# Performance work log

Measured on AMD Instinct MI355X. Metric: run time of the kernel, lower is better.

## Reference

```python
import jax, jax.numpy as jnp
import numpy as np

VOCAB = 100000
EMB = 100
HID = 100
CTX_LEN = 60          # must equal MAX_DESC_LEN for linear_1 to fit
FACT_LEN = 20
DESC_LEN = 60


def setup_inputs() -> dict:
    key = jax.random.key(0)
    ks = jax.random.split(key, 12)
    s = 0.05
    context = jax.random.randint(ks[0], (CTX_LEN, FACT_LEN), 1, VOCAB)
    fact_lengths = jax.random.randint(ks[1], (CTX_LEN,), 1, FACT_LEN)
    description = jax.random.randint(ks[2], (DESC_LEN,), 1, VOCAB)
    emb_ctx = jax.random.normal(ks[3], (VOCAB, EMB), jnp.float32) * s
    emb_ctx = emb_ctx.at[0].set(0.0)  # padding_idx=0
    emb_dec = jax.random.normal(ks[4], (VOCAB, EMB), jnp.float32) * s
    emb_dec = emb_dec.at[0].set(0.0)
    w1 = jax.random.normal(ks[5], (HID, CTX_LEN * HID), jnp.float32) * s
    b1 = jax.random.normal(ks[6], (HID,), jnp.float32) * s
    w_ih = jax.random.normal(ks[7], (3 * HID, EMB), jnp.float32) * s
    w_hh = jax.random.normal(ks[8], (3 * HID, HID), jnp.float32) * s
    b_ih = jax.random.normal(ks[9], (3 * HID,), jnp.float32) * s
    b_hh = jax.random.normal(ks[10], (3 * HID,), jnp.float32) * s
    w_out = jax.random.normal(ks[11], (VOCAB, HID), jnp.float32) * s
    b_out = jnp.zeros((VOCAB,), jnp.float32)
    return {"context": context, "fact_lengths": fact_lengths, "description": description,
            "emb_ctx": emb_ctx, "emb_dec": emb_dec, "w1": w1, "b1": b1,
            "w_ih": w_ih, "w_hh": w_hh, "b_ih": b_ih, "b_hh": b_hh,
            "w_out": w_out, "b_out": b_out}


def _forward(context, description, emb_ctx, emb_dec, w1, b1,
             w_ih, w_hh, b_ih, b_hh, w_out, b_out):
    # ---- InputModule: embed + positional fact encoder ----
    emb = emb_ctx[context]                       # [CTX_LEN, FACT_LEN, EMB]
    slen, elen = FACT_LEN, EMB
    s = jnp.arange(slen, dtype=jnp.float32) / (slen - 1)   # [slen]
    e = jnp.arange(elen, dtype=jnp.float32) / (elen - 1)   # [elen]
    l = 1.0 - s[:, None] - e[None, :] * (1.0 - 2.0 * s[:, None])  # [slen, elen]
    facts = jnp.sum(emb * l[None], axis=1)       # [CTX_LEN, EMB]

    # ---- initial decoder hidden from flattened facts ----
    h0 = facts.reshape(1, -1) @ w1.T + b1        # [1, HID]

    x0 = emb_dec[1][None, :]                     # SOS token embedding [1, EMB]

    def step(carry, tok):
        h, x = carry
        gi = x @ w_ih.T + b_ih                   # [1, 3H]
        gh = h @ w_hh.T + b_hh
        i_r, i_z, i_n = jnp.split(gi, 3, axis=-1)
        h_r, h_z, h_n = jnp.split(gh, 3, axis=-1)
        r = jax.nn.sigmoid(i_r + h_r)
        z = jax.nn.sigmoid(i_z + h_z)
        n = jnp.tanh(i_n + r * h_n)
        h_new = (1.0 - z) * n + z * h            # [1, HID]
        logits = h_new @ w_out.T + b_out         # [1, VOCAB]
        logp = jax.nn.log_softmax(logits, axis=-1)
        loss_t = -logp[0, tok]                   # NLLLoss, batch 1
        x_next = emb_dec[tok][None, :]           # teacher forcing
        return (h_new, x_next), loss_t

    (_, _), losses = jax.lax.scan(step, (h0, x0), description)
    return jnp.sum(losses).reshape(1)            # matches torch FloatTensor([.])


def reference(context, fact_lengths, description, emb_ctx, emb_dec, w1, b1,
              w_ih, w_hh, b_ih, b_hh, w_out, b_out):
    # fact_lengths is unused by the original forward (PositionalFactEncoder ignores it)
    return _forward(context, description, emb_ctx, emb_dec, w1, b1,
                    w_ih, w_hh, b_ih, b_hh, w_out, b_out)
```

## Files before the change

kernel.cpp:

```cpp
#include <hip/hip_runtime.h>
#include <hip/hip_bf16.h>
#include <math.h>

#define VOCAB 100000
#define EMB 100
#define HID 100
#define CTX_LEN 60
#define FACT_LEN 20
#define DESC_LEN 60
#define NCHUNK (VOCAB / 16)
#define GRID_BC 224
#define NWAVES_C (GRID_BC * 4)

#define WS_H0    0
#define WS_GI    128
#define WS_H     18176
#define WS_MS    24256
#define WS_WBF   262144

typedef __attribute__((ext_vector_type(8))) short short8;
typedef __attribute__((ext_vector_type(4))) float f32x4;

static __device__ __forceinline__ unsigned short f2bf(float f) {
    union { float f; unsigned u; } x; x.f = f;
    unsigned r = (x.u + 0x7FFFu + ((x.u >> 16) & 1u)) >> 16;
    return (unsigned short)r;
}

__global__ __launch_bounds__(320) void kA(const int* __restrict__ context,
                                          const int* __restrict__ desc,
                                          const float* __restrict__ emb_ctx,
                                          const float* __restrict__ emb_dec,
                                          const float* __restrict__ w1,
                                          const float* __restrict__ b1,
                                          const float* __restrict__ w_ih,
                                          const float* __restrict__ b_ih,
                                          float* __restrict__ ws,
                                          float* __restrict__ out) {
    const int b = blockIdx.x, tid = threadIdx.x;
    if (b < 100) {
        __shared__ int toks[1200];
        __shared__ float facts[6000];
        __shared__ float red[320];
        for (int i = tid; i < 1200; i += 320) toks[i] = context[i];
        __syncthreads();
        for (int idx = tid; idx < 6000; idx += 320) {
            int fb = idx / 100, e = idx - fb * 100;
            float ef = e * (1.f / 99.f);
            float acc = 0.f;
            #pragma unroll
            for (int s = 0; s < 20; s++) {
                float sf = s * (1.f / 19.f);
                float l = 1.f - sf - ef * (1.f - 2.f * sf);
                acc = fmaf(emb_ctx[toks[fb * 20 + s] * 100 + e], l, acc);
            }
            facts[idx] = acc;
        }
        __syncthreads();
        const float* wr = w1 + b * 6000;
        float p = 0.f;
        for (int k = tid; k < 6000; k += 320) p = fmaf(facts[k], wr[k], p);
        red[tid] = p; __syncthreads();
        if (tid < 64) red[tid] += red[256 + tid];
        __syncthreads();
        for (int st = 128; st > 0; st >>= 1) {
            if (tid < st) red[tid] += red[tid + st];
            __syncthreads();
        }
        if (tid == 0) ws[WS_H0 + b] = red[0] + b1[b];
    } else {
        const int t = b - 100;
        const int tok = (t == 0) ? 1 : desc[t - 1];
        __shared__ float xs[100];
        if (tid < 100) xs[tid] = emb_dec[tok * 100 + tid];
        __syncthreads();
        if (tid < 300) {
            float p = b_ih[tid];
            const float* wr = w_ih + tid * 100;
            #pragma unroll 4
            for (int k = 0; k < 100; k++) p = fmaf(wr[k], xs[k], p);
            ws[WS_GI + t * 300 + tid] = p;
        }
        if (b == 100 && tid == 319) out[0] = 0.f;
    }
}

__global__ __launch_bounds__(256, 1) void kB(const float* __restrict__ w_hh,
                                             const float* __restrict__ b_hh,
                                             const float* __restrict__ w_out,
                                             float* __restrict__ ws) {
    __shared__ __align__(16) float smem[24128];
    const int b = blockIdx.x, tid = threadIdx.x;
    const int lane = tid & 63, wave = tid >> 6;
    const int q = lane >> 4, n = lane & 15;

    if (b != 0) {
        short8* wbf = (short8*)(ws + WS_WBF);
        for (int it = (b - 1) * 4 + wave; it < NCHUNK * 4; it += 223 * 4) {
            int c = it >> 2, kt = it & 3;
            const float* wr = w_out + (c * 16 + n) * 100;
            int k0 = kt * 32 + q * 8;
            float va[8];
            #pragma unroll
            for (int jj = 0; jj < 8; jj++) va[jj] = 0.f;
            if (k0 + 4 <= 100) {
                float4 a = *(const float4*)(wr + k0);
                va[0] = a.x; va[1] = a.y; va[2] = a.z; va[3] = a.w;
            }
            if (k0 + 8 <= 100) {
                float4 a = *(const float4*)(wr + k0 + 4);
                va[4] = a.x; va[5] = a.y; va[6] = a.z; va[7] = a.w;
            }
            short8 f;
            #pragma unroll
            for (int jj = 0; jj < 8; jj++) f[jj] = (short)f2bf(va[jj]);
            wbf[(c * 4 + kt) * 64 + lane] = f;
        }
        return;
    }

    float* gi_lds = smem;
    float* H_lds  = smem + 18000;
    unsigned short (*h_bf)[128] = (unsigned short (*)[128])(smem + 24000);
    const int L = lane & 31;
    const int j = wave * 32 + L;
    const bool gate_lane = (lane < 32) && (j < 100);
    const bool w3skip = (wave == 3);

    short8 bfr[3][2][4];
    #pragma unroll
    for (int s = 0; s < 3; s++) {
        #pragma unroll
        for (int c = 0; c < 2; c++) {
            const int jrow = wave * 32 + c * 16 + n;
            const float* wr = w_hh + (s * 100 + jrow) * 100;
            #pragma unroll
            for (int kt = 0; kt < 4; kt++) {
                int k0 = kt * 32 + q * 8;
                float va[8];
                #pragma unroll
                for (int jj = 0; jj < 8; jj++) va[jj] = 0.f;
                if (jrow < 100) {
                    if (k0 + 4 <= 100) {
                        float4 a = *(const float4*)(wr + k0);
                        va[0] = a.x; va[1] = a.y; va[2] = a.z; va[3] = a.w;
                    }
                    if (k0 + 8 <= 100) {
                        float4 a = *(const float4*)(wr + k0 + 4);
                        va[4] = a.x; va[5] = a.y; va[6] = a.z; va[7] = a.w;
                    }
                }
                short8 f;
                #pragma unroll
                for (int jj = 0; jj < 8; jj++) f[jj] = (short)f2bf(va[jj]);
                bfr[s][c][kt] = f;
            }
        }
    }

    {
        const float4* src = (const float4*)(ws + WS_GI);
        float4* dst = (float4*)gi_lds;
        for (int k = tid; k < 4500; k += 256) dst[k] = src[k];
    }

    float hreg = 0.f, bh0 = 0.f, bh1 = 0.f, bh2 = 0.f;
    if (gate_lane) {
        hreg = ws[WS_H0 + j];
        bh0 = b_hh[j]; bh1 = b_hh[100 + j]; bh2 = b_hh[200 + j];
    }
    if (tid < 128) {
        h_bf[0][tid] = (tid < 100) ? f2bf(ws[WS_H0 + tid]) : (unsigned short)0;
        h_bf[1][tid] = 0;
    }
    __syncthreads();

    const int js = (j < 100) ? j : 0;
    float gir = gi_lds[js];
    float giz = gi_lds[100 + js];
    float gin = gi_lds[200 + js];

    for (int t = 0; t < 60; t++) {
        const int rb = t & 1;

        short8 afr[4];
        #pragma unroll
        for (int kt = 0; kt < 4; kt++)
            afr[kt] = *(const short8*)&h_bf[rb][kt * 32 + q * 8];

        const int tn = (t < 59) ? (t + 1) * 300 : 59 * 300;
        float gir_n = gi_lds[tn + js];
        float giz_n = gi_lds[tn + 100 + js];
        float gin_n = gi_lds[tn + 200 + js];

        f32x4 acc[3][2];
        #pragma unroll
        for (int s = 0; s < 3; s++) {
            #pragma unroll
            for (int c = 0; c < 2; c++) {
                f32x4 a = {0.f, 0.f, 0.f, 0.f};
                if (c == 0 || !w3skip) {
                    a = __builtin_amdgcn_mfma_f32_16x16x32_bf16(afr[0], bfr[s][c][0], a, 0, 0, 0);
                    a = __builtin_amdgcn_mfma_f32_16x16x32_bf16(afr[1], bfr[s][c][1], a, 0, 0, 0);
                    a = __builtin_amdgcn_mfma_f32_16x16x32_bf16(afr[2], bfr[s][c][2], a, 0, 0, 0);
                    a = __builtin_amdgcn_mfma_f32_16x16x32_bf16(afr[3], bfr[s][c][3], a, 0, 0, 0);
                }
                acc[s][c] = a;
            }
        }

        if (gate_lane) {
            const int cc = L >> 4;
            float ghr = (cc ? acc[0][1][0] : acc[0][0][0]) + bh0;
            float ghz = (cc ? acc[1][1][0] : acc[1][0][0]) + bh1;
            float ghn = (cc ? acc[2][1][0] : acc[2][0][0]) + bh2;
            float r = 1.f / (1.f + __expf(-(gir + ghr)));
            float z = 1.f / (1.f + __expf(-(giz + ghz)));
            float a2 = fmaf(r, ghn, gin);
            float tt = __expf(-2.f * fabsf(a2));
            float nn = copysignf((1.f - tt) / (1.f + tt), a2);
            hreg = (1.f - z) * nn + z * hreg;
            h_bf[rb ^ 1][j] = f2bf(hreg);
            H_lds[t * 100 + j] = hreg;
        }
        gir = gir_n; giz = giz_n; gin = gin_n;
        __syncthreads();
    }

    {
        const float4* src = (const float4*)H_lds;
        float4* dst = (float4*)(ws + WS_H);
        for (int k = tid; k < 1500; k += 256) dst[k] = src[k];
    }
}

__global__ __launch_bounds__(256, 1) void kC(const float* __restrict__ b_out,
                                             float* __restrict__ ws) {
    const float* H = ws + WS_H;
    float* ms = ws + WS_MS;
    const short8* wbf = (const short8*)(ws + WS_WBF);
    const int tid = threadIdx.x;
    const int lane = tid & 63, wave = tid >> 6;
    const int q = lane >> 4, n = lane & 15;
    const int gw = blockIdx.x * 4 + wave;
    const int k_base = q * 8;

    short8 afr[4][4];
    #pragma unroll
    for (int mt = 0; mt < 4; mt++) {
        int m = mt * 16 + n;
        #pragma unroll
        for (int kt = 0; kt < 4; kt++) {
            int k0 = kt * 32 + k_base;
            float va[8];
            #pragma unroll
            for (int jj = 0; jj < 8; jj++) va[jj] = 0.f;
            if (m < 60) {
                if (k0 + 4 <= 100) {
                    float4 a = *(const float4*)(H + m * 100 + k0);
                    va[0] = a.x; va[1] = a.y; va[2] = a.z; va[3] = a.w;
                }
                if (k0 + 8 <= 100) {
                    float4 a = *(const float4*)(H + m * 100 + k0 + 4);
                    va[4] = a.x; va[5] = a.y; va[6] = a.z; va[7] = a.w;
                }
            }
            short8 f;
            #pragma unroll
            for (int jj = 0; jj < 8; jj++) f[jj] = (short)f2bf(va[jj]);
            afr[mt][kt] = f;
        }
    }

    float mS[16], sS[16];
    #pragma unroll
    for (int i = 0; i < 16; i++) { mS[i] = -3.0e38f; sS[i] = 0.f; }

    for (int c = gw; c < NCHUNK; c += NWAVES_C) {
        int row = c * 16 + n;
        short8 bw0 = wbf[(c * 4 + 0) * 64 + lane];
        short8 bw1 = wbf[(c * 4 + 1) * 64 + lane];
        short8 bw2 = wbf[(c * 4 + 2) * 64 + lane];
        short8 bw3 = wbf[(c * 4 + 3) * 64 + lane];
        float bo = b_out[row];
        #pragma unroll
        for (int mt = 0; mt < 4; mt++) {
            f32x4 acc = {0.f, 0.f, 0.f, 0.f};
            acc = __builtin_amdgcn_mfma_f32_16x16x32_bf16(afr[mt][0], bw0, acc, 0, 0, 0);
            acc = __builtin_amdgcn_mfma_f32_16x16x32_bf16(afr[mt][1], bw1, acc, 0, 0, 0);
            acc = __builtin_amdgcn_mfma_f32_16x16x32_bf16(afr[mt][2], bw2, acc, 0, 0, 0);
            acc = __builtin_amdgcn_mfma_f32_16x16x32_bf16(afr[mt][3], bw3, acc, 0, 0, 0);
            #pragma unroll
            for (int reg = 0; reg < 4; reg++) {
                float x = acc[reg] + bo;
                int i = mt * 4 + reg;
                float mo = mS[i];
                float mn = fmaxf(mo, x);
                sS[i] = sS[i] * __expf(mo - mn) + __expf(x - mn);
                mS[i] = mn;
            }
        }
    }

    #pragma unroll
    for (int i = 0; i < 16; i++) {
        float m = mS[i], s = sS[i];
        #pragma unroll
        for (int off = 1; off < 16; off <<= 1) {
            float m2 = __shfl_xor(m, off);
            float s2 = __shfl_xor(s, off);
            float mn = fmaxf(m, m2);
            s = s * __expf(m - mn) + s2 * __expf(m2 - mn);
            m = mn;
        }
        mS[i] = m; sS[i] = s;
    }
    if (n == 0) {
        #pragma unroll
        for (int mt = 0; mt < 4; mt++) {
            #pragma unroll
            for (int reg = 0; reg < 4; reg++) {
                int t = mt * 16 + q * 4 + reg;
                int i = mt * 4 + reg;
                if (t < 60) {
                    float2 val; val.x = mS[i]; val.y = sS[i];
                    ((float2*)ms)[t * NWAVES_C + gw] = val;
                }
            }
        }
    }
}

__global__ __launch_bounds__(256) void kD(const int* __restrict__ desc,
                                          const float* __restrict__ w_out,
                                          const float* __restrict__ b_out,
                                          const float* __restrict__ ws,
                                          float* __restrict__ out) {
    const int t = blockIdx.x, tid = threadIdx.x;
    __shared__ float sm[256], ss[256], sd[256];
    const float2* msp = (const float2*)(ws + WS_MS);
    float m = -3.0e38f, s = 0.f;
    for (int i = tid; i < NWAVES_C; i += 256) {
        float2 p2 = msp[t * NWAVES_C + i];
        float mn = fmaxf(m, p2.x);
        s = s * __expf(m - mn) + p2.y * __expf(p2.x - mn);
        m = mn;
    }
    sm[tid] = m; ss[tid] = s; __syncthreads();
    for (int st = 128; st > 0; st >>= 1) {
        if (tid < st) {
            float mo = sm[tid], so = ss[tid];
            float m2 = sm[tid + st], s2 = ss[tid + st];
            float mn = fmaxf(mo, m2);
            sm[tid] = mn;
            ss[tid] = so * __expf(mo - mn) + s2 * __expf(m2 - mn);
        }
        __syncthreads();
    }
    const int tok = desc[t];
    float p = 0.f;
    if (tid < 100) p = ws[WS_H + t * 100 + tid] * w_out[tok * 100 + tid];
    sd[tid] = p; __syncthreads();
    for (int st = 128; st > 0; st >>= 1) {
        if (tid < st) sd[tid] += sd[tid + st];
        __syncthreads();
    }
    if (tid == 0) {
        float logit = sd[0] + b_out[tok];
        atomicAdd(out, sm[0] + logf(ss[0]) - logit);
    }
}

extern "C" void kernel_launch(void* const* d_in, const int* in_sizes, int n_in,
                              void* d_out, int out_size, void* d_ws, size_t ws_size,
                              hipStream_t stream) {
    const int*   context = (const int*)d_in[0];
    const int*   desc    = (const int*)d_in[2];
    const float* emb_ctx = (const float*)d_in[3];
    const float* emb_dec = (const float*)d_in[4];
    const float* w1      = (const float*)d_in[5];
    const float* b1      = (const float*)d_in[6];
    const float* w_ih    = (const float*)d_in[7];
    const float* w_hh    = (const float*)d_in[8];
    const float* b_ih    = (const float*)d_in[9];
    const float* b_hh    = (const float*)d_in[10];
    const float* w_out   = (const float*)d_in[11];
    const float* b_out   = (const float*)d_in[12];
    float* out = (float*)d_out;
    float* ws  = (float*)d_ws;

    kA<<<160, 320, 0, stream>>>(context, desc, emb_ctx, emb_dec, w1, b1, w_ih, b_ih, ws, out);
    kB<<<GRID_BC, 256, 0, stream>>>(w_hh, b_hh, w_out, ws);
    kC<<<GRID_BC, 256, 0, stream>>>(b_out, ws);
    kD<<<60, 256, 0, stream>>>(desc, w_out, b_out, ws, out);
}
```

Baseline: 203.8 us.

## Fuse GRU recurrence and vocab projection into one persistent kernel with flag handoff

Merges the GRU recurrence kernel and the output-projection/logsumexp kernel into a single launch. Non-leader blocks keep their bf16-converted w_out chunks in registers and spin on a global flag that block 0 releases once the hidden states are written. This removes the bf16 weight round-trip through workspace and one kernel launch, and overlaps loading the weights with the serial recurrence. It relies on all 224 blocks being co-resident, since the spin-wait would deadlock otherwise, and it raises register pressure by holding 7 chunks per wave.

New measurement: 206.2 us. About the same (+1.2%).

```diff
diff --git a/kernel.cpp b/kernel.cpp
--- a/kernel.cpp
+++ b/kernel.cpp
@@ -9,14 +9,15 @@
 #define FACT_LEN 20
 #define DESC_LEN 60
 #define NCHUNK (VOCAB / 16)
-#define GRID_BC 224
-#define NWAVES_C (GRID_BC * 4)
-
-#define WS_H0    0
-#define WS_GI    128
-#define WS_H     18176
+#define GRID_B 224
+#define NWAVES_C (GRID_B * 4)
+#define CPW 7
+
+#define WS_FLAG  0
+#define WS_H0    64
+#define WS_GI    192
+#define WS_H     18192
 #define WS_MS    24256
-#define WS_WBF   262144
 
 typedef __attribute__((ext_vector_type(8))) short short8;
 typedef __attribute__((ext_vector_type(4))) float f32x4;
@@ -25,6 +26,17 @@
     union { float f; unsigned u; } x; x.f = f;
     unsigned r = (x.u + 0x7FFFu + ((x.u >> 16) & 1u)) >> 16;
     return (unsigned short)r;
+}
+
+static __device__ __forceinline__ void release_flag(float* ws) {
+    __builtin_amdgcn_fence(__ATOMIC_RELEASE, "agent");
+    __hip_atomic_store((unsigned*)ws + WS_FLAG, 1u, __ATOMIC_RELAXED, __HIP_MEMORY_SCOPE_AGENT);
+}
+static __device__ __forceinline__ void wait_flag(const float* ws) {
+    while (__hip_atomic_load((const unsigned*)ws + WS_FLAG, __ATOMIC_RELAXED,
+                             __HIP_MEMORY_SCOPE_AGENT) == 0u)
+        __builtin_amdgcn_s_sleep(16);
+    __builtin_amdgcn_fence(__ATOMIC_ACQUIRE, "agent");
 }
 
 __global__ __launch_bounds__(320) void kA(const int* __restrict__ context,
@@ -81,6 +93,7 @@
             for (int k = 0; k < 100; k++) p = fmaf(wr[k], xs[k], p);
             ws[WS_GI + t * 300 + tid] = p;
         }
+        if (b == 100 && tid == 318) ((unsigned*)ws)[WS_FLAG] = 0u;
         if (b == 100 && tid == 319) out[0] = 0.f;
     }
 }
@@ -88,59 +101,28 @@
 __global__ __launch_bounds__(256, 1) void kB(const float* __restrict__ w_hh,
                                              const float* __restrict__ b_hh,
                                              const float* __restrict__ w_out,
+                                             const float* __restrict__ b_out,
                                              float* __restrict__ ws) {
     __shared__ __align__(16) float smem[24128];
     const int b = blockIdx.x, tid = threadIdx.x;
     const int lane = tid & 63, wave = tid >> 6;
     const int q = lane >> 4, n = lane & 15;
+    const int gw = b * 4 + wave;
+
+    short8 bw[CPW][4];
 
     if (b != 0) {
-        short8* wbf = (short8*)(ws + WS_WBF);
-        for (int it = (b - 1) * 4 + wave; it < NCHUNK * 4; it += 223 * 4) {
-            int c = it >> 2, kt = it & 3;
-            const float* wr = w_out + (c * 16 + n) * 100;
-            int k0 = kt * 32 + q * 8;
-            float va[8];
-            #pragma unroll
-            for (int jj = 0; jj < 8; jj++) va[jj] = 0.f;
-            if (k0 + 4 <= 100) {
-                float4 a = *(const float4*)(wr + k0);
-                va[0] = a.x; va[1] = a.y; va[2] = a.z; va[3] = a.w;
-            }
-            if (k0 + 8 <= 100) {
-                float4 a = *(const float4*)(wr + k0 + 4);
-                va[4] = a.x; va[5] = a.y; va[6] = a.z; va[7] = a.w;
-            }
-            short8 f;
-            #pragma unroll
-            for (int jj = 0; jj < 8; jj++) f[jj] = (short)f2bf(va[jj]);
-            wbf[(c * 4 + kt) * 64 + lane] = f;
-        }
-        return;
-    }
-
-    float* gi_lds = smem;
-    float* H_lds  = smem + 18000;
-    unsigned short (*h_bf)[128] = (unsigned short (*)[128])(smem + 24000);
-    const int L = lane & 31;
-    const int j = wave * 32 + L;
-    const bool gate_lane = (lane < 32) && (j < 100);
-    const bool w3skip = (wave == 3);
-
-    short8 bfr[3][2][4];
-    #pragma unroll
-    for (int s = 0; s < 3; s++) {
-        #pragma unroll
-        for (int c = 0; c < 2; c++) {
-            const int jrow = wave * 32 + c * 16 + n;
-            const float* wr = w_hh + (s * 100 + jrow) * 100;
-            #pragma unroll
-            for (int kt = 0; kt < 4; kt++) {
-                int k0 = kt * 32 + q * 8;
-                float va[8];
-                #pragma unroll
-                for (int jj = 0; jj < 8; jj++) va[jj] = 0.f;
-                if (jrow < 100) {
+        #pragma unroll
+        for (int k = 0; k < CPW; k++) {
+            int c = gw + k * NWAVES_C;
+            if (c < NCHUNK) {
+                const float* wr = w_out + (c * 16 + n) * 100;
+                #pragma unroll
+                for (int kt = 0; kt < 4; kt++) {
+                    int k0 = kt * 32 + q * 8;
+                    float va[8];
+                    #pragma unroll
+                    for (int jj = 0; jj < 8; jj++) va[jj] = 0.f;
                     if (k0 + 4 <= 100) {
                         float4 a = *(const float4*)(wr + k0);
                         va[0] = a.x; va[1] = a.y; va[2] = a.z; va[3] = a.w;
@@ -149,182 +131,236 @@
                         float4 a = *(const float4*)(wr + k0 + 4);
                         va[4] = a.x; va[5] = a.y; va[6] = a.z; va[7] = a.w;
                     }
-                }
-                short8 f;
-                #pragma unroll
-                for (int jj = 0; jj < 8; jj++) f[jj] = (short)f2bf(va[jj]);
-                bfr[s][c][kt] = f;
-            }
-        }
-    }
-
-    {
-        const float4* src = (const float4*)(ws + WS_GI);
-        float4* dst = (float4*)gi_lds;
-        for (int k = tid; k < 4500; k += 256) dst[k] = src[k];
-    }
-
-    float hreg = 0.f, bh0 = 0.f, bh1 = 0.f, bh2 = 0.f;
-    if (gate_lane) {
-        hreg = ws[WS_H0 + j];
-        bh0 = b_hh[j]; bh1 = b_hh[100 + j]; bh2 = b_hh[200 + j];
-    }
-    if (tid < 128) {
-        h_bf[0][tid] = (tid < 100) ? f2bf(ws[WS_H0 + tid]) : (unsigned short)0;
-        h_bf[1][tid] = 0;
-    }
-    __syncthreads();
-
-    const int js = (j < 100) ? j : 0;
-    float gir = gi_lds[js];
-    float giz = gi_lds[100 + js];
-    float gin = gi_lds[200 + js];
-
-    for (int t = 0; t < 60; t++) {
-        const int rb = t & 1;
-
-        short8 afr[4];
-        #pragma unroll
-        for (int kt = 0; kt < 4; kt++)
-            afr[kt] = *(const short8*)&h_bf[rb][kt * 32 + q * 8];
-
-        const int tn = (t < 59) ? (t + 1) * 300 : 59 * 300;
-        float gir_n = gi_lds[tn + js];
-        float giz_n = gi_lds[tn + 100 + js];
-        float gin_n = gi_lds[tn + 200 + js];
-
-        f32x4 acc[3][2];
+                    short8 f;
+                    #pragma unroll
+                    for (int jj = 0; jj < 8; jj++) f[jj] = (short)f2bf(va[jj]);
+                    bw[k][kt] = f;
+                }
+            }
+        }
+        if (tid == 0) wait_flag(ws);
+        __syncthreads();
+    } else {
+        float* gi_lds = smem;
+        float* H_lds  = smem + 18000;
+        unsigned short (*h_bf)[128] = (unsigned short (*)[128])(smem + 24000);
+        const int L = lane & 31;
+        const int j = wave * 32 + L;
+        const bool gate_lane = (lane < 32) && (j < 100);
+
+        short8 bfr[3][2][4];
         #pragma unroll
         for (int s = 0; s < 3; s++) {
             #pragma unroll
             for (int c = 0; c < 2; c++) {
-                f32x4 a = {0.f, 0.f, 0.f, 0.f};
-                if (c == 0 || !w3skip) {
+                const int jrow = wave * 32 + c * 16 + n;
+                const float* wr = w_hh + (s * 100 + jrow) * 100;
+                #pragma unroll
+                for (int kt = 0; kt < 4; kt++) {
+                    int k0 = kt * 32 + q * 8;
+                    float va[8];
+                    #pragma unroll
+                    for (int jj = 0; jj < 8; jj++) va[jj] = 0.f;
+                    if (jrow < 100) {
+                        if (k0 + 4 <= 100) {
+                            float4 a = *(const float4*)(wr + k0);
+                            va[0] = a.x; va[1] = a.y; va[2] = a.z; va[3] = a.w;
+                        }
+                        if (k0 + 8 <= 100) {
+                            float4 a = *(const float4*)(wr + k0 + 4);
+                            va[4] = a.x; va[5] = a.y; va[6] = a.z; va[7] = a.w;
+                        }
+                    }
+                    short8 f;
+                    #pragma unroll
+                    for (int jj = 0; jj < 8; jj++) f[jj] = (short)f2bf(va[jj]);
+                    bfr[s][c][kt] = f;
+                }
+            }
+        }
+
+        {
+            const float4* src = (const float4*)(ws + WS_GI);
+            float4* dst = (float4*)gi_lds;
+            for (int k = tid; k < 4500; k += 256) dst[k] = src[k];
+        }
+
+        float hreg = 0.f, bh0 = 0.f, bh1 = 0.f, bh2 = 0.f;
+        if (gate_lane) {
+            hreg = ws[WS_H0 + j];
+            bh0 = b_hh[j]; bh1 = b_hh[100 + j]; bh2 = b_hh[200 + j];
+        }
+        if (tid < 128) {
+            h_bf[0][tid] = (tid < 100) ? f2bf(ws[WS_H0 + tid]) : (unsigned short)0;
+            h_bf[1][tid] = 0;
+        }
+        __syncthreads();
+
+        const int js = (j < 100) ? j : 0;
+        for (int t = 0; t < 60; t++) {
+            const int rb = t & 1;
+            float gir = gi_lds[t * 300 + js];
+            float giz = gi_lds[t * 300 + 100 + js];
+            float gin = gi_lds[t * 300 + 200 + js];
+
+            short8 afr[4];
+            #pragma unroll
+            for (int kt = 0; kt < 4; kt++)
+                afr[kt] = *(const short8*)&h_bf[rb][kt * 32 + q * 8];
+
+            f32x4 acc[3][2];
+            #pragma unroll
+            for (int s = 0; s < 3; s++) {
+                #pragma unroll
+                for (int c = 0; c < 2; c++) {
+                    f32x4 a = {0.f, 0.f, 0.f, 0.f};
                     a = __builtin_amdgcn_mfma_f32_16x16x32_bf16(afr[0], bfr[s][c][0], a, 0, 0, 0);
                     a = __builtin_amdgcn_mfma_f32_16x16x32_bf16(afr[1], bfr[s][c][1], a, 0, 0, 0);
                     a = __builtin_amdgcn_mfma_f32_16x16x32_bf16(afr[2], bfr[s][c][2], a, 0, 0, 0);
                     a = __builtin_amdgcn_mfma_f32_16x16x32_bf16(afr[3], bfr[s][c][3], a, 0, 0, 0);
-                }
-                acc[s][c] = a;
-            }
-        }
-
-        if (gate_lane) {
-            const int cc = L >> 4;
-            float ghr = (cc ? acc[0][1][0] : acc[0][0][0]) + bh0;
-            float ghz = (cc ? acc[1][1][0] : acc[1][0][0]) + bh1;
-            float ghn = (cc ? acc[2][1][0] : acc[2][0][0]) + bh2;
-            float r = 1.f / (1.f + __expf(-(gir + ghr)));
-            float z = 1.f / (1.f + __expf(-(giz + ghz)));
-            float a2 = fmaf(r, ghn, gin);
-            float tt = __expf(-2.f * fabsf(a2));
-            float nn = copysignf((1.f - tt) / (1.f + tt), a2);
-            hreg = (1.f - z) * nn + z * hreg;
-            h_bf[rb ^ 1][j] = f2bf(hreg);
-            H_lds[t * 100 + j] = hreg;
-        }
-        gir = gir_n; giz = giz_n; gin = gin_n;
-        __syncthreads();
+                    acc[s][c] = a;
+                }
+            }
+
+            if (gate_lane) {
+                const int cc = L >> 4;
+                float ghr = (cc ? acc[0][1][0] : acc[0][0][0]) + bh0;
+                float ghz = (cc ? acc[1][1][0] : acc[1][0][0]) + bh1;
+                float ghn = (cc ? acc[2][1][0] : acc[2][0][0]) + bh2;
+                float r = 1.f / (1.f + __expf(-(gir + ghr)));
+                float z = 1.f / (1.f + __expf(-(giz + ghz)));
+                float a2 = fmaf(r, ghn, gin);
+                float tt = __expf(-2.f * fabsf(a2));
+                float nn = copysignf((1.f - tt) / (1.f + tt), a2);
+                hreg = (1.f - z) * nn + z * hreg;
+                h_bf[rb ^ 1][j] = f2bf(hreg);
+                H_lds[t * 100 + j] = hreg;
+            }
+            __syncthreads();
+        }
+
+        {
+            const float4* src = (const float4*)H_lds;
+            float4* dst = (float4*)(ws + WS_H);
+            for (int k = tid; k < 1500; k += 256) dst[k] = src[k];
+        }
+        __syncthreads();
+        if (tid == 0) release_flag(ws);
+
+        #pragma unroll
+        for (int k = 0; k < CPW; k++) {
+            int c = gw + k * NWAVES_C;
+            if (c < NCHUNK) {
+                const float* wr = w_out + (c * 16 + n) * 100;
+                #pragma unroll
+                for (int kt = 0; kt < 4; kt++) {
+                    int k0 = kt * 32 + q * 8;
+                    float va[8];
+                    #pragma unroll
+                    for (int jj = 0; jj < 8; jj++) va[jj] = 0.f;
+                    if (k0 + 4 <= 100) {
+                        float4 a = *(const float4*)(wr + k0);
+                        va[0] = a.x; va[1] = a.y; va[2] = a.z; va[3] = a.w;
+                    }
+                    if (k0 + 8 <= 100) {
+                        float4 a = *(const float4*)(wr + k0 + 4);
+                        va[4] = a.x; va[5] = a.y; va[6] = a.z; va[7] = a.w;
+                    }
+                    short8 f;
+                    #pragma unroll
+                    for (int jj = 0; jj < 8; jj++) f[jj] = (short)f2bf(va[jj]);
+                    bw[k][kt] = f;
+                }
+            }
+        }
     }
 
     {
-        const float4* src = (const float4*)H_lds;
-        float4* dst = (float4*)(ws + WS_H);
-        for (int k = tid; k < 1500; k += 256) dst[k] = src[k];
-    }
-}
-
-__global__ __launch_bounds__(256, 1) void kC(const float* __restrict__ b_out,
-                                             float* __restrict__ ws) {
-    const float* H = ws + WS_H;
-    float* ms = ws + WS_MS;
-    const short8* wbf = (const short8*)(ws + WS_WBF);
-    const int tid = threadIdx.x;
-    const int lane = tid & 63, wave = tid >> 6;
-    const int q = lane >> 4, n = lane & 15;
-    const int gw = blockIdx.x * 4 + wave;
-    const int k_base = q * 8;
-
-    short8 afr[4][4];
-    #pragma unroll
-    for (int mt = 0; mt < 4; mt++) {
-        int m = mt * 16 + n;
-        #pragma unroll
-        for (int kt = 0; kt < 4; kt++) {
-            int k0 = kt * 32 + k_base;
-            float va[8];
-            #pragma unroll
-            for (int jj = 0; jj < 8; jj++) va[jj] = 0.f;
-            if (m < 60) {
-                if (k0 + 4 <= 100) {
-                    float4 a = *(const float4*)(H + m * 100 + k0);
-                    va[0] = a.x; va[1] = a.y; va[2] = a.z; va[3] = a.w;
-                }
-                if (k0 + 8 <= 100) {
-                    float4 a = *(const float4*)(H + m * 100 + k0 + 4);
-                    va[4] = a.x; va[5] = a.y; va[6] = a.z; va[7] = a.w;
-                }
-            }
-            short8 f;
-            #pragma unroll
-            for (int jj = 0; jj < 8; jj++) f[jj] = (short)f2bf(va[jj]);
-            afr[mt][kt] = f;
-        }
-    }
-
-    float mS[16], sS[16];
-    #pragma unroll
-    for (int i = 0; i < 16; i++) { mS[i] = -3.0e38f; sS[i] = 0.f; }
-
-    for (int c = gw; c < NCHUNK; c += NWAVES_C) {
-        int row = c * 16 + n;
-        short8 bw0 = wbf[(c * 4 + 0) * 64 + lane];
-        short8 bw1 = wbf[(c * 4 + 1) * 64 + lane];
-        short8 bw2 = wbf[(c * 4 + 2) * 64 + lane];
-        short8 bw3 = wbf[(c * 4 + 3) * 64 + lane];
-        float bo = b_out[row];
+        const float* H = ws + WS_H;
+        float* ms = ws + WS_MS;
+        const int k_base = q * 8;
+
+        short8 afr[4][4];
         #pragma unroll
         for (int mt = 0; mt < 4; mt++) {
-            f32x4 acc = {0.f, 0.f, 0.f, 0.f};
-            acc = __builtin_amdgcn_mfma_f32_16x16x32_bf16(afr[mt][0], bw0, acc, 0, 0, 0);
-            acc = __builtin_amdgcn_mfma_f32_16x16x32_bf16(afr[mt][1], bw1, acc, 0, 0, 0);
-            acc = __builtin_amdgcn_mfma_f32_16x16x32_bf16(afr[mt][2], bw2, acc, 0, 0, 0);
-            acc = __builtin_amdgcn_mfma_f32_16x16x32_bf16(afr[mt][3], bw3, acc, 0, 0, 0);
-            #pragma unroll
-            for (int reg = 0; reg < 4; reg++) {
-                float x = acc[reg] + bo;
-                int i = mt * 4 + reg;
-                float mo = mS[i];
-                float mn = fmaxf(mo, x);
-                sS[i] = sS[i] * __expf(mo - mn) + __expf(x - mn);
-                mS[i] = mn;
-            }
-        }
-    }
-
-    #pragma unroll
-    for (int i = 0; i < 16; i++) {
-        float m = mS[i], s = sS[i];
-        #pragma unroll
-        for (int off = 1; off < 16; off <<= 1) {
-            float m2 = __shfl_xor(m, off);
-            float s2 = __shfl_xor(s, off);
-            float mn = fmaxf(m, m2);
-            s = s * __expf(m - mn) + s2 * __expf(m2 - mn);
-            m = mn;
-        }
-        mS[i] = m; sS[i] = s;
-    }
-    if (n == 0) {
-        #pragma unroll
-        for (int mt = 0; mt < 4; mt++) {
-            #pragma unroll
-            for (int reg = 0; reg < 4; reg++) {
-                int t = mt * 16 + q * 4 + reg;
-                int i = mt * 4 + reg;
-                if (t < 60) {
-                    float2 val; val.x = mS[i]; val.y = sS[i];
-                    ((float2*)ms)[t * NWAVES_C + gw] = val;
+            int m = mt * 16 + n;
+            #pragma unroll
+            for (int kt = 0; kt < 4; kt++) {
+                int k0 = kt * 32 + k_base;
+                float va[8];
+                #pragma unroll
+                for (int jj = 0; jj < 8; jj++) va[jj] = 0.f;
+                if (m < 60) {
+                    if (k0 + 4 <= 100) {
+                        float4 a = *(const float4*)(H + m * 100 + k0);
+                        va[0] = a.x; va[1] = a.y; va[2] = a.z; va[3] = a.w;
+                    }
+                    if (k0 + 8 <= 100) {
+                        float4 a = *(const float4*)(H + m * 100 + k0 + 4);
+                        va[4] = a.x; va[5] = a.y; va[6] = a.z; va[7] = a.w;
+                    }
+                }
+                short8 f;
+                #pragma unroll
+                for (int jj = 0; jj < 8; jj++) f[jj] = (short)f2bf(va[jj]);
+                afr[mt][kt] = f;
+            }
+        }
+
+        float mS[16], sS[16];
+        #pragma unroll
+        for (int i = 0; i < 16; i++) { mS[i] = -3.0e38f; sS[i] = 0.f; }
+
+        #pragma unroll
+        for (int k = 0; k < CPW; k++) {
+            int c = gw + k * NWAVES_C;
+            if (c < NCHUNK) {
+                int row = c * 16 + n;
+                float bo = b_out[row];
+                #pragma unroll
+                for (int mt = 0; mt < 4; mt++) {
+                    f32x4 acc = {0.f, 0.f, 0.f, 0.f};
+                    acc = __builtin_amdgcn_mfma_f32_16x16x32_bf16(afr[mt][0], bw[k][0], acc, 0, 0, 0);
+                    acc = __builtin_amdgcn_mfma_f32_16x16x32_bf16(afr[mt][1], bw[k][1], acc, 0, 0, 0);
+                    acc = __builtin_amdgcn_mfma_f32_16x16x32_bf16(afr[mt][2], bw[k][2], acc, 0, 0, 0);
+                    acc = __builtin_amdgcn_mfma_f32_16x16x32_bf16(afr[mt][3], bw[k][3], acc, 0, 0, 0);
+                    #pragma unroll
+                    for (int reg = 0; reg < 4; reg++) {
+                        float x = acc[reg] + bo;
+                        int i = mt * 4 + reg;
+                        float mo = mS[i];
+                        float mn = fmaxf(mo, x);
+                        sS[i] = sS[i] * __expf(mo - mn) + __expf(x - mn);
+                        mS[i] = mn;
+                    }
+                }
+            }
+        }
+
+        #pragma unroll
+        for (int i = 0; i < 16; i++) {
+            float m = mS[i], s = sS[i];
+            #pragma unroll
+            for (int off = 1; off < 16; off <<= 1) {
+                float m2 = __shfl_xor(m, off);
+                float s2 = __shfl_xor(s, off);
+                float mn = fmaxf(m, m2);
+                s = s * __expf(m - mn) + s2 * __expf(m2 - mn);
+                m = mn;
+            }
+            mS[i] = m; sS[i] = s;
+        }
+        if (n == 0) {
+            #pragma unroll
+            for (int mt = 0; mt < 4; mt++) {
+                #pragma unroll
+                for (int reg = 0; reg < 4; reg++) {
+                    int t = mt * 16 + q * 4 + reg;
+                    int i = mt * 4 + reg;
+                    if (t < 60) {
+                        float2 val; val.x = mS[i]; val.y = sS[i];
+                        ((float2*)ms)[t * NWAVES_C + gw] = val;
+                    }
                 }
             }
         }
@@ -390,7 +426,6 @@
     float* ws  = (float*)d_ws;
 
     kA<<<160, 320, 0, stream>>>(context, desc, emb_ctx, emb_dec, w1, b1, w_ih, b_ih, ws, out);
-    kB<<<GRID_BC, 256, 0, stream>>>(w_hh, b_hh, w_out, ws);
-    kC<<<GRID_BC, 256, 0, stream>>>(b_out, ws);
+    kB<<<GRID_B, 256, 0, stream>>>(w_hh, b_hh, w_out, b_out, ws);
     kD<<<60, 256, 0, stream>>>(desc, w_out, b_out, ws, out);
 }
```
